# Performance work log

Measured on AMD Instinct MI355X. Metric: run time of the kernel, lower is better.

## Reference

```python
import jax, jax.numpy as jnp
import numpy as np

PROJ = 8192     # projDim
THRESH = 1e-8   # numerical-stability epsilon for signed sqrt
L2_EPS = 1e-12  # eps of torch F.normalize


def setup_inputs() -> dict:
    key = jax.random.key(0)
    k1, k2, k3, k4, k5 = jax.random.split(key, 5)
    B, C, H, W = 16, 512, 14, 14
    x = jax.random.normal(k1, (B, C, H, W), dtype=jnp.float32)
    h1 = jax.random.randint(k2, (C,), 0, PROJ, dtype=jnp.int32)
    h2 = jax.random.randint(k3, (C,), 0, PROJ, dtype=jnp.int32)
    s1 = (2 * jax.random.randint(k4, (C,), 0, 2) - 1).astype(jnp.float32)
    s2 = (2 * jax.random.randint(k5, (C,), 0, 2) - 1).astype(jnp.float32)
    return {"x": x, "s1": s1, "s2": s2, "h1": h1, "h2": h2}


def reference(x, s1, s2, h1, h2):
    # x: [B, C, H, W]; h*: [C] hash buckets in [0, PROJ); s*: [C] signs (+-1)
    B, C, H, W = x.shape
    x_flat = jnp.transpose(x, (0, 2, 3, 1)).reshape(-1, C)  # [N, C], N = B*H*W

    def count_sketch(s, h):
        # Equivalent to x_flat @ M with M[c, h[c]] = s[c]: scatter-add of
        # sign-weighted channels into PROJ bins.  -> [N, PROJ]
        return jax.ops.segment_sum((x_flat * s).T, h, num_segments=PROJ).T

    fft1 = jnp.fft.fft(count_sketch(s1, h1), axis=-1)
    fft2 = jnp.fft.fft(count_sketch(s2, h2), axis=-1)
    conv = jnp.fft.ifft(fft1 * fft2, axis=-1).real       # [N, PROJ]
    y = conv.reshape(B, H, W, PROJ).sum(axis=(1, 2))      # sum pool -> [B, PROJ]
    y = jnp.sign(y) * jnp.sqrt(jnp.abs(y) + THRESH)       # signed sqrt
    norm = jnp.linalg.norm(y, axis=1, keepdims=True)
    return y / jnp.maximum(norm, L2_EPS)                  # l2 normalize (dim=1)
```

## Files before the change

### kernel.cpp

```cpp
#include <hip/hip_runtime.h>
#include <math.h>

#define PROJ 8192
#define NB   16
#define NC   512
#define HW   196
#define KP   224
#define XELE ((size_t)NB * NC * KP)

typedef __attribute__((ext_vector_type(8))) short bf16x8;
typedef __attribute__((ext_vector_type(4))) short short4v;
typedef __attribute__((ext_vector_type(4))) float f32x4;

__device__ __forceinline__ unsigned bf16_rne(float f) {
    unsigned u = __builtin_bit_cast(unsigned, f);
    return (u + 0x7fffu + ((u >> 16) & 1u)) >> 16;
}

__global__ __launch_bounds__(256)
void cbp_prep(const float* __restrict__ x,
              short* __restrict__ xh, short* __restrict__ xl) {
    const int id  = blockIdx.x * 256 + threadIdx.x;
    const int q   = id % 56;
    const int row = id / 56;
    float4 v = {0.f, 0.f, 0.f, 0.f};
    if (q < 49) v = *(const float4*)&x[(size_t)row * HW + 4 * q];
    const float f[4] = {v.x, v.y, v.z, v.w};
    short4v h, l;
#pragma unroll
    for (int c = 0; c < 4; ++c) {
        const unsigned hb = bf16_rne(f[c]);
        h[c] = (short)hb;
        l[c] = (short)bf16_rne(f[c] - __builtin_bit_cast(float, hb << 16));
    }
    *(short4v*)&xh[(size_t)row * KP + 4 * q] = h;
    *(short4v*)&xl[(size_t)row * KP + 4 * q] = l;
}

#define LOADFRAGS(buf, kc)                                          \
    {                                                               \
        const int off_ = (kc) * 32;                                 \
        ah[buf][0] = *(const bf16x8*)&pAh[off_];                    \
        ah[buf][1] = *(const bf16x8*)&pAh[16 * KP + off_];          \
        al[buf][0] = *(const bf16x8*)&pAl[off_];                    \
        al[buf][1] = *(const bf16x8*)&pAl[16 * KP + off_];          \
        bh[buf][0] = *(const bf16x8*)&pBh[off_];                    \
        bh[buf][1] = *(const bf16x8*)&pBh[16 * KP + off_];          \
        bl[buf][0] = *(const bf16x8*)&pBl[off_];                    \
        bl[buf][1] = *(const bf16x8*)&pBl[16 * KP + off_];          \
    }

__global__ __launch_bounds__(1024)
void cbp_gram(const short* __restrict__ xh, const short* __restrict__ xl,
              const float* __restrict__ s1, const float* __restrict__ s2,
              const int*   __restrict__ h1, const int*   __restrict__ h2,
              float* __restrict__ partials) {
    __shared__ float sk[PROJ];

    const int tid = threadIdx.x;
    const int blk = blockIdx.x;
    const int xcd = blk & 7;
    const int sub = blk >> 3;
    const int hi  = sub >> 4;
    const int q   = sub & 15;
    const int b   = 2 * xcd + hi;

    for (int i = tid; i < PROJ; i += 1024) sk[i] = 0.f;
    __syncthreads();

    const int wave = tid >> 6, lane = tid & 63;
    const int quad = lane >> 4, l15 = lane & 15;
    const int tile = q * 4 + (wave >> 2);
    const int I = tile >> 3, J = tile & 7;
    const int qr = ((wave >> 1) & 1) * 32;
    const int qc = (wave & 1) * 32;
    const int c1 = I * 64 + qr;
    const int c2 = J * 64 + qc;

    const size_t rowA = ((size_t)b * NC + c1 + l15) * KP + quad * 8;
    const size_t rowB = ((size_t)b * NC + c2 + l15) * KP + quad * 8;
    const short* pAh = xh + rowA;  const short* pAl = xl + rowA;
    const short* pBh = xh + rowB;  const short* pBl = xl + rowB;

    f32x4 acc[2][2];
#pragma unroll
    for (int i = 0; i < 2; ++i)
#pragma unroll
        for (int j = 0; j < 2; ++j) acc[i][j] = (f32x4){0.f, 0.f, 0.f, 0.f};

    bf16x8 ah[2][2], al[2][2], bh[2][2], bl[2][2];
    LOADFRAGS(0, 0)
#pragma unroll
    for (int kc = 0; kc < 7; ++kc) {
        const int cur = kc & 1;
        if (kc < 6) LOADFRAGS(cur ^ 1, kc + 1)
#pragma unroll
        for (int i = 0; i < 2; ++i)
#pragma unroll
            for (int j = 0; j < 2; ++j) {
                acc[i][j] = __builtin_amdgcn_mfma_f32_16x16x32_bf16(ah[cur][i], bh[cur][j], acc[i][j], 0, 0, 0);
                acc[i][j] = __builtin_amdgcn_mfma_f32_16x16x32_bf16(ah[cur][i], bl[cur][j], acc[i][j], 0, 0, 0);
                acc[i][j] = __builtin_amdgcn_mfma_f32_16x16x32_bf16(al[cur][i], bh[cur][j], acc[i][j], 0, 0, 0);
            }
    }

    int   ha[2][4], hb[2];
    float sa[2][4], sb[2];
#pragma unroll
    for (int i = 0; i < 2; ++i) {
        const int r0 = c1 + i * 16 + quad * 4;
#pragma unroll
        for (int rg = 0; rg < 4; ++rg) {
            ha[i][rg] = h1[r0 + rg];
            sa[i][rg] = s1[r0 + rg];
        }
    }
#pragma unroll
    for (int j = 0; j < 2; ++j) {
        const int c = c2 + j * 16 + l15;
        hb[j] = h2[c];
        sb[j] = s2[c];
    }
#pragma unroll
    for (int i = 0; i < 2; ++i)
#pragma unroll
        for (int j = 0; j < 2; ++j)
#pragma unroll
            for (int rg = 0; rg < 4; ++rg) {
                const int bin = (ha[i][rg] + hb[j]) & (PROJ - 1);
                atomicAdd(&sk[bin], sa[i][rg] * sb[j] * acc[i][j][rg]);
            }
    __syncthreads();

    float4* dst = (float4*)(partials + (size_t)blk * PROJ);
    const float4* src = (const float4*)sk;
    for (int i = tid; i < PROJ / 4; i += 1024) dst[i] = src[i];
}

__global__ __launch_bounds__(256)
void cbp_reduce(const float* __restrict__ partials, float* __restrict__ y,
                float* __restrict__ ssqp) {
    const int blk = blockIdx.x;
    const int xcd = blk & 7;
    const int k   = blk >> 3;
    const int hi  = k >> 5;
    const int seg = k & 31;
    const int b   = 2 * xcd + hi;
    const int tid = threadIdx.x;
    const int bin = seg * 256 + tid;

    float s = 0.f;
#pragma unroll
    for (int u = 0; u < 16; ++u) {
        const int u2 = (u + seg) & 15;
        const int pb = ((hi * 16 + u2) << 3) | xcd;
        s += partials[(size_t)pb * PROJ + bin];
    }

    const float m = sqrtf(fabsf(s) + 1e-8f);
    const float o = (s > 0.f) ? m : (s < 0.f ? -m : 0.f);
    y[b * PROJ + bin] = o;

    __shared__ float red[256];
    red[tid] = o * o;
    __syncthreads();
#pragma unroll
    for (int st = 128; st >= 1; st >>= 1) {
        if (tid < st) red[tid] += red[tid + st];
        __syncthreads();
    }
    if (tid == 0) ssqp[blk] = red[0];
}

__global__ __launch_bounds__(256)
void cbp_normalize(float* __restrict__ y, const float* __restrict__ ssqp) {
    const int b   = blockIdx.x >> 1;
    const int off = (blockIdx.x & 1) * 4096;
    const int tid = threadIdx.x;
    float ssq = 0.f;
#pragma unroll
    for (int seg = 0; seg < 32; ++seg)
        ssq += ssqp[(((b & 1) * 32 + seg) << 3) | (b >> 1)];
    const float inv = 1.0f / fmaxf(sqrtf(ssq), 1e-12f);

    float4* row = (float4*)&y[(size_t)b * PROJ + off];
#pragma unroll
    for (int j = 0; j < 4; ++j) {
        float4 v = row[j * 256 + tid];
        v.x *= inv; v.y *= inv; v.z *= inv; v.w *= inv;
        row[j * 256 + tid] = v;
    }
}

extern "C" void kernel_launch(void* const* d_in, const int* in_sizes, int n_in,
                              void* d_out, int out_size, void* d_ws, size_t ws_size,
                              hipStream_t stream) {
    const float* x  = (const float*)d_in[0];
    const float* s1 = (const float*)d_in[1];
    const float* s2 = (const float*)d_in[2];
    const int*   h1 = (const int*)d_in[3];
    const int*   h2 = (const int*)d_in[4];
    float* y = (float*)d_out;

    short* xh = (short*)d_ws;
    short* xl = xh + XELE;
    float* partials = (float*)(xl + XELE);
    float* ssqp = partials + (size_t)256 * PROJ;

    hipLaunchKernelGGL(cbp_prep, dim3(1792), dim3(256), 0, stream, x, xh, xl);
    hipLaunchKernelGGL(cbp_gram, dim3(256), dim3(1024), 0, stream,
                       xh, xl, s1, s2, h1, h2, partials);
    hipLaunchKernelGGL(cbp_reduce, dim3(512), dim3(256), 0, stream,
                       partials, y, ssqp);
    hipLaunchKernelGGL(cbp_normalize, dim3(32), dim3(256), 0, stream, y, ssqp);
}
```

Measured before the change: 108.2 us.

## Stage Gram tiles through LDS with 128x128 block tiles and cached hashes

The Gram kernel now gives each block a single 128x128 channel tile instead of four 64x64 tiles. Operand fragments are staged cooperatively through padded shared memory and prefetched into registers one k-chunk ahead. The hash and sign vectors are loaded once into shared memory. Each wave computes a 32x64 sub-tile with more MFMAs per fragment load, and the block size drops to 512 threads with two blocks per CU. This is meant to cut redundant global loads of the same rows across waves, at the cost of two barriers per k-step and more LDS use.

```diff
diff --git a/kernel.cpp b/kernel.cpp
--- a/kernel.cpp
+++ b/kernel.cpp
@@ -6,6 +6,7 @@
 #define NC   512
 #define HW   196
 #define KP   224
+#define LST  40
 #define XELE ((size_t)NB * NC * KP)
 
 typedef __attribute__((ext_vector_type(8))) short bf16x8;
@@ -37,104 +38,118 @@
     *(short4v*)&xl[(size_t)row * KP + 4 * q] = l;
 }
 
-#define LOADFRAGS(buf, kc)                                          \
-    {                                                               \
-        const int off_ = (kc) * 32;                                 \
-        ah[buf][0] = *(const bf16x8*)&pAh[off_];                    \
-        ah[buf][1] = *(const bf16x8*)&pAh[16 * KP + off_];          \
-        al[buf][0] = *(const bf16x8*)&pAl[off_];                    \
-        al[buf][1] = *(const bf16x8*)&pAl[16 * KP + off_];          \
-        bh[buf][0] = *(const bf16x8*)&pBh[off_];                    \
-        bh[buf][1] = *(const bf16x8*)&pBh[16 * KP + off_];          \
-        bl[buf][0] = *(const bf16x8*)&pBl[off_];                    \
-        bl[buf][1] = *(const bf16x8*)&pBl[16 * KP + off_];          \
-    }
-
-__global__ __launch_bounds__(1024)
+__global__ __launch_bounds__(512, 2)
 void cbp_gram(const short* __restrict__ xh, const short* __restrict__ xl,
               const float* __restrict__ s1, const float* __restrict__ s2,
               const int*   __restrict__ h1, const int*   __restrict__ h2,
               float* __restrict__ partials) {
     __shared__ float sk[PROJ];
+    __shared__ short Ah[128 * LST];
+    __shared__ short Al[128 * LST];
+    __shared__ short Bh[128 * LST];
+    __shared__ short Bl[128 * LST];
+    __shared__ int   lh1[128], lh2[128];
+    __shared__ float ls1[128], ls2[128];
 
     const int tid = threadIdx.x;
     const int blk = blockIdx.x;
     const int xcd = blk & 7;
-    const int sub = blk >> 3;
-    const int hi  = sub >> 4;
-    const int q   = sub & 15;
+    const int hi  = blk >> 7;
     const int b   = 2 * xcd + hi;
-
-    for (int i = tid; i < PROJ; i += 1024) sk[i] = 0.f;
-    __syncthreads();
+    const int tile = (blk >> 3) & 15;
+    const int I = tile >> 2, J = tile & 3;
+    const int c1base = I * 128, c2base = J * 128;
+
+    for (int i = tid; i < PROJ; i += 512) sk[i] = 0.f;
+    if (tid < 128) {
+        lh1[tid] = h1[c1base + tid];  ls1[tid] = s1[c1base + tid];
+    } else if (tid < 256) {
+        const int t = tid - 128;
+        lh2[t] = h2[c2base + t];  ls2[t] = s2[c2base + t];
+    }
 
     const int wave = tid >> 6, lane = tid & 63;
     const int quad = lane >> 4, l15 = lane & 15;
-    const int tile = q * 4 + (wave >> 2);
-    const int I = tile >> 3, J = tile & 7;
-    const int qr = ((wave >> 1) & 1) * 32;
-    const int qc = (wave & 1) * 32;
-    const int c1 = I * 64 + qr;
-    const int c2 = J * 64 + qc;
-
-    const size_t rowA = ((size_t)b * NC + c1 + l15) * KP + quad * 8;
-    const size_t rowB = ((size_t)b * NC + c2 + l15) * KP + quad * 8;
-    const short* pAh = xh + rowA;  const short* pAl = xl + rowA;
-    const short* pBh = xh + rowB;  const short* pBl = xl + rowB;
-
-    f32x4 acc[2][2];
+    const int wr = (wave >> 1) * 32;
+    const int wc = (wave & 1) * 64;
+
+    const int sr = tid >> 2;
+    const int sl = tid & 3;
+
+    const size_t baseA = ((size_t)b * NC + c1base + sr) * KP + sl * 8;
+    const size_t baseB = ((size_t)b * NC + c2base + sr) * KP + sl * 8;
+
+    bf16x8 pAh, pAl, pBh, pBl;
+    pAh = *(const bf16x8*)&xh[baseA];
+    pAl = *(const bf16x8*)&xl[baseA];
+    pBh = *(const bf16x8*)&xh[baseB];
+    pBl = *(const bf16x8*)&xl[baseB];
+
+    f32x4 acc[2][4];
 #pragma unroll
     for (int i = 0; i < 2; ++i)
 #pragma unroll
-        for (int j = 0; j < 2; ++j) acc[i][j] = (f32x4){0.f, 0.f, 0.f, 0.f};
-
-    bf16x8 ah[2][2], al[2][2], bh[2][2], bl[2][2];
-    LOADFRAGS(0, 0)
-#pragma unroll
+        for (int j = 0; j < 4; ++j) acc[i][j] = (f32x4){0.f, 0.f, 0.f, 0.f};
+
     for (int kc = 0; kc < 7; ++kc) {
-        const int cur = kc & 1;
-        if (kc < 6) LOADFRAGS(cur ^ 1, kc + 1)
+        __syncthreads();
+        *(bf16x8*)&Ah[sr * LST + sl * 8] = pAh;
+        *(bf16x8*)&Al[sr * LST + sl * 8] = pAl;
+        *(bf16x8*)&Bh[sr * LST + sl * 8] = pBh;
+        *(bf16x8*)&Bl[sr * LST + sl * 8] = pBl;
+        if (kc < 6) {
+            const size_t off = (size_t)(kc + 1) * 32;
+            pAh = *(const bf16x8*)&xh[baseA + off];
+            pAl = *(const bf16x8*)&xl[baseA + off];
+            pBh = *(const bf16x8*)&xh[baseB + off];
+            pBl = *(const bf16x8*)&xl[baseB + off];
+        }
+        __syncthreads();
+
+        bf16x8 ahf[2], alf[2], bhf[4], blf[4];
+#pragma unroll
+        for (int i = 0; i < 2; ++i) {
+            const int ra = wr + i * 16 + l15;
+            ahf[i] = *(const bf16x8*)&Ah[ra * LST + quad * 8];
+            alf[i] = *(const bf16x8*)&Al[ra * LST + quad * 8];
+        }
+#pragma unroll
+        for (int j = 0; j < 4; ++j) {
+            const int rb = wc + j * 16 + l15;
+            bhf[j] = *(const bf16x8*)&Bh[rb * LST + quad * 8];
+            blf[j] = *(const bf16x8*)&Bl[rb * LST + quad * 8];
+        }
 #pragma unroll
         for (int i = 0; i < 2; ++i)
 #pragma unroll
-            for (int j = 0; j < 2; ++j) {
-                acc[i][j] = __builtin_amdgcn_mfma_f32_16x16x32_bf16(ah[cur][i], bh[cur][j], acc[i][j], 0, 0, 0);
-                acc[i][j] = __builtin_amdgcn_mfma_f32_16x16x32_bf16(ah[cur][i], bl[cur][j], acc[i][j], 0, 0, 0);
-                acc[i][j] = __builtin_amdgcn_mfma_f32_16x16x32_bf16(al[cur][i], bh[cur][j], acc[i][j], 0, 0, 0);
+            for (int j = 0; j < 4; ++j) {
+                acc[i][j] = __builtin_amdgcn_mfma_f32_16x16x32_bf16(ahf[i], bhf[j], acc[i][j], 0, 0, 0);
+                acc[i][j] = __builtin_amdgcn_mfma_f32_16x16x32_bf16(ahf[i], blf[j], acc[i][j], 0, 0, 0);
+                acc[i][j] = __builtin_amdgcn_mfma_f32_16x16x32_bf16(alf[i], bhf[j], acc[i][j], 0, 0, 0);
             }
     }
 
-    int   ha[2][4], hb[2];
-    float sa[2][4], sb[2];
 #pragma unroll
     for (int i = 0; i < 2; ++i) {
-        const int r0 = c1 + i * 16 + quad * 4;
-#pragma unroll
-        for (int rg = 0; rg < 4; ++rg) {
-            ha[i][rg] = h1[r0 + rg];
-            sa[i][rg] = s1[r0 + rg];
-        }
-    }
-#pragma unroll
-    for (int j = 0; j < 2; ++j) {
-        const int c = c2 + j * 16 + l15;
-        hb[j] = h2[c];
-        sb[j] = s2[c];
-    }
-#pragma unroll
-    for (int i = 0; i < 2; ++i)
-#pragma unroll
-        for (int j = 0; j < 2; ++j)
+        const int r0 = wr + i * 16 + quad * 4;
+#pragma unroll
+        for (int j = 0; j < 4; ++j) {
+            const int c = wc + j * 16 + l15;
+            const int h2v = lh2[c];
+            const float s2v = ls2[c];
 #pragma unroll
             for (int rg = 0; rg < 4; ++rg) {
-                const int bin = (ha[i][rg] + hb[j]) & (PROJ - 1);
-                atomicAdd(&sk[bin], sa[i][rg] * sb[j] * acc[i][j][rg]);
+                const int r = r0 + rg;
+                const int bin = (lh1[r] + h2v) & (PROJ - 1);
+                atomicAdd(&sk[bin], ls1[r] * s2v * acc[i][j][rg]);
             }
+        }
+    }
     __syncthreads();
 
     float4* dst = (float4*)(partials + (size_t)blk * PROJ);
     const float4* src = (const float4*)sk;
-    for (int i = tid; i < PROJ / 4; i += 1024) dst[i] = src[i];
+    for (int i = tid; i < PROJ / 4; i += 512) dst[i] = src[i];
 }
 
 __global__ __launch_bounds__(256)
@@ -153,7 +168,7 @@
 #pragma unroll
     for (int u = 0; u < 16; ++u) {
         const int u2 = (u + seg) & 15;
-        const int pb = ((hi * 16 + u2) << 3) | xcd;
+        const int pb = xcd | (u2 << 3) | (hi << 7);
         s += partials[(size_t)pb * PROJ + bin];
     }
 
@@ -208,7 +223,7 @@
     float* ssqp = partials + (size_t)256 * PROJ;
 
     hipLaunchKernelGGL(cbp_prep, dim3(1792), dim3(256), 0, stream, x, xh, xl);
-    hipLaunchKernelGGL(cbp_gram, dim3(256), dim3(1024), 0, stream,
+    hipLaunchKernelGGL(cbp_gram, dim3(256), dim3(512), 0, stream,
                        xh, xl, s1, s2, h1, h2, partials);
     hipLaunchKernelGGL(cbp_reduce, dim3(512), dim3(256), 0, stream,
                        partials, y, ssqp);
```

Result: faster. 105.4 us (-2.7%).
